# Optimization experiments

Measured on AMD Instinct MI355X. Metric: run time of the kernel, lower is better.

The kernel has to match this reference:

```python
import jax, jax.numpy as jnp
import numpy as np

B, N, DX, E, H, HD, KH, FF = 8, 8192, 2, 128, 8, 16, 32, 128
G1, G2, PMAX = 32, 32, 32


def _ln(x, g, b):
    mu = jnp.mean(x, axis=-1, keepdims=True)
    var = jnp.mean((x - mu) ** 2, axis=-1, keepdims=True)
    return (x - mu) * jax.lax.rsqrt(var + 1e-5) * g + b


def _cumcount_row(idx):
    # for each element, number of earlier elements with the same value (stable)
    n = idx.shape[0]
    order = jnp.argsort(idx)  # stable
    si = idx[order]
    ar = jnp.arange(n)
    is_start = jnp.concatenate([jnp.ones((1,), bool), si[1:] != si[:-1]])
    seg_start = jax.lax.associative_scan(jnp.maximum, jnp.where(is_start, ar, 0))
    return jnp.zeros(n, jnp.int32).at[order].set((ar - seg_start).astype(jnp.int32))


def _forward(x, z, latent, Wq, Wk, Wv, Wo, bo, kW1, kb1, kW2, kb2,
             lnq_g, lnq_b, lnk_g, lnk_b, ln2_g, ln2_b, fW1, fb1, fW2, fb2,
             grid_n1, grid_n2, max_patch, num_heads):
    Bb, Nn, dx = x.shape
    e = latent.shape[0]
    dims = (grid_n1, grid_n2)
    M = grid_n1 * grid_n2
    P = max_patch
    h = num_heads
    hd = Wq.shape[1] // h
    # grid range from data (margin = 0), regular grid via linspace
    mins = [jnp.min(x[:, :, i]) for i in range(dx)]
    maxs = [jnp.max(x[:, :, i]) for i in range(dx)]
    axes = [jnp.linspace(mins[i], maxs[i], dims[i]) for i in range(dx)]
    x_grid = jnp.stack(jnp.meshgrid(*axes, indexing="ij"), axis=-1)  # [G1,G2,dx]
    x_grid_flat = x_grid.reshape(M, dx)
    # nearest grid cell per point: regular grid -> per-dim rounding
    flat = None
    for i in range(dx):
        step = (maxs[i] - mins[i]) / (dims[i] - 1)
        ii = jnp.clip(jnp.round((x[..., i] - mins[i]) / step), 0, dims[i] - 1).astype(jnp.int32)
        flat = ii if flat is None else flat * dims[i] + ii
    cell = flat  # [B,N]
    cumc = jax.vmap(_cumcount_row)(cell)          # slot within cell
    slot = jnp.where(cumc < P, cumc, P)           # overflow -> dummy slot (dropped)
    bidx = jnp.broadcast_to(jnp.arange(Bb)[:, None], (Bb, Nn))
    # scatter points into per-cell padded neighbour sets [B, M, P, d]
    jx = jnp.zeros((Bb, M, P + 1, dx), x.dtype).at[bidx, cell, slot].set(x)[:, :, :P]
    jz = jnp.zeros((Bb, M, P + 1, e), z.dtype).at[bidx, cell, slot].set(z)[:, :, :P]
    msk = jnp.zeros((Bb, M, P + 1), bool).at[bidx, cell, slot].set(True)[:, :, :P]
    xg = jnp.broadcast_to(x_grid_flat[None], (Bb, M, dx))
    zg = jnp.broadcast_to(latent[None, None, :], (Bb, M, e))
    # concatenate_x_grid=True: grid token prepended, always attended
    joint_x = jnp.concatenate([xg[:, :, None, :], jx], axis=2).reshape(Bb * M, P + 1, dx)
    joint_z = jnp.concatenate([zg[:, :, None, :], jz], axis=2).reshape(Bb * M, P + 1, e)
    att_mask = jnp.concatenate([jnp.ones((Bb, M, 1), bool), msk], axis=2).reshape(Bb * M, P + 1)
    xq = xg.reshape(Bb * M, 1, dx)
    zq = zg.reshape(Bb * M, 1, e)
    T = Bb * M
    # masked translation-equivariant cross-attention (pre-norm layer)
    q = jnp.einsum("tqe,ef->tqf", _ln(zq, lnq_g, lnq_b), Wq).reshape(T, 1, h, hd)
    zk_n = _ln(joint_z, lnk_g, lnk_b)
    k = jnp.einsum("tke,ef->tkf", zk_n, Wk).reshape(T, P + 1, h, hd)
    v = jnp.einsum("tke,ef->tkf", zk_n, Wv).reshape(T, P + 1, h, hd)
    dots = jnp.einsum("tqhd,tkhd->thqk", q, k) / jnp.sqrt(jnp.asarray(hd, q.dtype))
    diff = joint_x[:, None, :, :] - xq[:, :, None, :]            # [T,1,P+1,dx]
    kb = jnp.maximum(diff @ kW1 + kb1, 0.0) @ kW2 + kb2          # kernel bias [T,1,P+1,h]
    dots = dots + jnp.transpose(kb, (0, 3, 1, 2))
    dots = jnp.where(att_mask[:, None, None, :], dots, -1e9)
    A = jax.nn.softmax(dots, axis=-1)                            # [T,h,1,P+1]
    out = jnp.einsum("thqk,tkhd->tqhd", A, v).reshape(T, 1, h * hd)
    z_new = zq + out @ Wo + bo
    z_new = z_new + (jnp.maximum(_ln(z_new, ln2_g, ln2_b) @ fW1 + fb1, 0.0) @ fW2 + fb2)
    x_new = jnp.einsum("tqk,tkd->tqd", jnp.mean(A, axis=1), joint_x)  # TE location update
    x_grid_out = x_new.reshape(Bb, grid_n1, grid_n2, dx)
    z_grid_out = z_new.reshape(Bb, grid_n1, grid_n2, e)
    return (x_grid_out, z_grid_out)


def setup_inputs():
    key = jax.random.key(0)
    ks = jax.random.split(key, 12)
    s = 0.05
    return {
        "x": jax.random.uniform(ks[0], (B, N, DX), jnp.float32),
        "z": jax.random.normal(ks[1], (B, N, E), jnp.float32),
        "grid_n1": G1, "grid_n2": G2, "max_patch": PMAX, "num_heads": H,
        "latent": jax.random.normal(ks[2], (E,), jnp.float32),
        "Wq": jax.random.normal(ks[3], (E, H * HD), jnp.float32) * s,
        "Wk": jax.random.normal(ks[4], (E, H * HD), jnp.float32) * s,
        "Wv": jax.random.normal(ks[5], (E, H * HD), jnp.float32) * s,
        "Wo": jax.random.normal(ks[6], (H * HD, E), jnp.float32) * s,
        "bo": jnp.zeros((E,), jnp.float32),
        "kW1": jax.random.normal(ks[7], (DX, KH), jnp.float32) * s,
        "kb1": jnp.zeros((KH,), jnp.float32),
        "kW2": jax.random.normal(ks[8], (KH, H), jnp.float32) * s,
        "kb2": jnp.zeros((H,), jnp.float32),
        "lnq_g": jnp.ones((E,), jnp.float32), "lnq_b": jnp.zeros((E,), jnp.float32),
        "lnk_g": jnp.ones((E,), jnp.float32), "lnk_b": jnp.zeros((E,), jnp.float32),
        "ln2_g": jnp.ones((E,), jnp.float32), "ln2_b": jnp.zeros((E,), jnp.float32),
        "fW1": jax.random.normal(ks[9], (E, FF), jnp.float32) * s,
        "fb1": jnp.zeros((FF,), jnp.float32),
        "fW2": jax.random.normal(ks[10], (FF, E), jnp.float32) * s,
        "fb2": jnp.zeros((E,), jnp.float32),
    }


def reference(x, z, grid_n1, grid_n2, max_patch, num_heads, latent, Wq, Wk, Wv, Wo, bo,
              kW1, kb1, kW2, kb2, lnq_g, lnq_b, lnk_g, lnk_b, ln2_g, ln2_b,
              fW1, fb1, fW2, fb2):
    return _forward(x, z, latent, Wq, Wk, Wv, Wo, bo, kW1, kb1, kW2, kb2,
                    lnq_g, lnq_b, lnk_g, lnk_b, ln2_g, ln2_b, fW1, fb1, fW2, fb2,
                    grid_n1, grid_n2, max_patch, num_heads)
```

## Files before the change

### kernel.cpp

```cpp
#include <hip/hip_runtime.h>
#include <stdint.h>

#define NB 8
#define NN 8192
#define NE 128
#define NH 8
#define NHD 16
#define NKH 32
#define NFF 128
#define NG 32
#define NM 1024
#define NP 32
#define NT 8192
#define NPTS 65536

typedef __attribute__((ext_vector_type(8))) short bf16x8_t;
typedef __attribute__((ext_vector_type(4))) float f32x4_t;

#define WS_MM      0
#define WS_D0      64
#define WS_Q       128
#define WS_VG      640
#define WS_PART    1152
#define WS_CNT     2048
#define WS_CELL    34816
#define WS_PIDX    296960
#define WS_WVT     1345536
#define WS_WOT     1411072
#define WS_FW1T    1443840
#define WS_FW2T    1476608
#define WS_WKQT    1509376
#define WS_SCORES  1513472
#define WS_KV      4194304

__device__ __forceinline__ unsigned short f2bf(float f) {
    unsigned u = __float_as_uint(f);
    u += 0x7FFFu + ((u >> 16) & 1u);
    return (unsigned short)(u >> 16);
}
__device__ __forceinline__ float bflo(unsigned w) { return __uint_as_float(w << 16); }
__device__ __forceinline__ float bfhi(unsigned w) { return __uint_as_float(w & 0xFFFF0000u); }

__global__ __launch_bounds__(256) void k_setup(
        const float* __restrict__ x,
        const float* __restrict__ Wk, const float* __restrict__ Wv, const float* __restrict__ Wo,
        const float* __restrict__ fW1, const float* __restrict__ fW2,
        const float* __restrict__ latent, const float* __restrict__ Wq,
        const float* __restrict__ lnq_g, const float* __restrict__ lnq_b,
        const float* __restrict__ lnk_g, const float* __restrict__ lnk_b,
        const float* __restrict__ kb1, const float* __restrict__ kW2, const float* __restrict__ kb2,
        int* __restrict__ cnt,
        unsigned short* __restrict__ WvT, unsigned short* __restrict__ WoT,
        unsigned short* __restrict__ fW1T, unsigned short* __restrict__ fW2T,
        float* __restrict__ ws_q, float* __restrict__ ws_vg, float* __restrict__ ws_d0,
        unsigned short* __restrict__ WkqT,
        float4* __restrict__ part) {
    int blk = blockIdx.x;
    int t = threadIdx.x;
    if (blk < 16) {
        __shared__ float s_t[64][65];
        const float* src; unsigned short* dst;
        int n0, k0;
        if (blk < 4) {
            int tn = blk >> 1, tk = blk & 1;
            n0 = tn * 64; k0 = tk * 64;
            src = Wv; dst = WvT;
        } else {
            int m = (blk - 4) >> 2, s4 = (blk - 4) & 3;
            int tn = s4 >> 1, tk = s4 & 1;
            n0 = tn * 64; k0 = tk * 64;
            src = (m == 0) ? Wo : (m == 1) ? fW1 : fW2;
            dst = (m == 0) ? WoT : (m == 1) ? fW1T : fW2T;
        }
        int tx = t & 63, ty = t >> 6;
        #pragma unroll
        for (int r = 0; r < 16; ++r) {
            int kr = r * 4 + ty;
            s_t[kr][tx] = src[(k0 + kr) * 128 + n0 + tx];
        }
        __syncthreads();
        #pragma unroll
        for (int r = 0; r < 16; ++r) {
            int nr = r * 4 + ty;
            dst[(n0 + nr) * 128 + k0 + tx] = f2bf(s_t[tx][nr]);
        }
    } else if (blk < 48) {
        int idx = (blk - 16) * 256 + t;
        cnt[idx] = 0;
    } else if (blk == 48) {
        __shared__ float s_qn[128], s_kn[128], s_q[128], s_kg[128];
        __shared__ float s_mu, s_rstd;
        if (t < 64) {
            float v0 = latent[t], v1 = latent[t + 64];
            float s = v0 + v1;
            for (int m = 32; m > 0; m >>= 1) s += __shfl_xor(s, m);
            float mu = s * (1.0f / 128.0f);
            float d0 = v0 - mu, d1 = v1 - mu;
            float q = d0 * d0 + d1 * d1;
            for (int m = 32; m > 0; m >>= 1) q += __shfl_xor(q, m);
            if (t == 0) { s_mu = mu; s_rstd = rsqrtf(q * (1.0f / 128.0f) + 1e-5f); }
        }
        __syncthreads();
        if (t < 128) {
            float nv = (latent[t] - s_mu) * s_rstd;
            s_qn[t] = nv * lnq_g[t] + lnq_b[t];
            s_kn[t] = nv * lnk_g[t] + lnk_b[t];
        }
        __syncthreads();
        if (t < 128) {
            float aq = 0.f, ak = 0.f, av = 0.f;
            for (int e = 0; e < 128; ++e) {
                aq += s_qn[e] * Wq[e * 128 + t];
                ak += s_kn[e] * Wk[e * 128 + t];
                av += s_kn[e] * Wv[e * 128 + t];
            }
            s_q[t] = aq; s_kg[t] = ak;
            ws_q[t] = aq; ws_vg[t] = av;
        }
        __syncthreads();
        if (t < 128) {
            const float* wr = Wk + t * 128;
            #pragma unroll
            for (int h = 0; h < 8; ++h) {
                float a = 0.f;
                #pragma unroll
                for (int d = 0; d < 16; ++d) a += wr[h * 16 + d] * s_q[h * 16 + d];
                WkqT[h * 128 + t] = f2bf(a * 0.25f);
                WkqT[(h + 8) * 128 + t] = 0;
            }
        }
        if (t < 8) {
            float acc = 0.f;
            for (int d = 0; d < 16; ++d) acc += s_q[t * 16 + d] * s_kg[t * 16 + d];
            float kb0 = kb2[t];
            for (int j = 0; j < 32; ++j) kb0 += fmaxf(kb1[j], 0.f) * kW2[j * 8 + t];
            ws_d0[t] = acc * 0.25f + kb0;
        }
    } else {
        __shared__ float s_red[4][4];
        int pb = blk - 49;
        const float4* xp = (const float4*)x + pb * 1024;
        float mn0 = 1e30f, mx0 = -1e30f, mn1 = 1e30f, mx1 = -1e30f;
        #pragma unroll
        for (int it = 0; it < 4; ++it) {
            float4 v = xp[it * 256 + t];
            mn0 = fminf(mn0, fminf(v.x, v.z)); mx0 = fmaxf(mx0, fmaxf(v.x, v.z));
            mn1 = fminf(mn1, fminf(v.y, v.w)); mx1 = fmaxf(mx1, fmaxf(v.y, v.w));
        }
        #pragma unroll
        for (int m = 32; m > 0; m >>= 1) {
            mn0 = fminf(mn0, __shfl_xor(mn0, m)); mx0 = fmaxf(mx0, __shfl_xor(mx0, m));
            mn1 = fminf(mn1, __shfl_xor(mn1, m)); mx1 = fmaxf(mx1, __shfl_xor(mx1, m));
        }
        int w = t >> 6;
        if ((t & 63) == 0) {
            s_red[w][0] = mn0; s_red[w][1] = mn1; s_red[w][2] = mx0; s_red[w][3] = mx1;
        }
        __syncthreads();
        if (t == 0) {
            float a0 = fminf(fminf(s_red[0][0], s_red[1][0]), fminf(s_red[2][0], s_red[3][0]));
            float a1 = fminf(fminf(s_red[0][1], s_red[1][1]), fminf(s_red[2][1], s_red[3][1]));
            float b0 = fmaxf(fmaxf(s_red[0][2], s_red[1][2]), fmaxf(s_red[2][2], s_red[3][2]));
            float b1 = fmaxf(fmaxf(s_red[0][3], s_red[1][3]), fmaxf(s_red[2][3], s_red[3][3]));
            part[pb] = make_float4(a0, a1, b0, b1);
        }
    }
}

__global__ __launch_bounds__(256) void k_binkv(
        const float* __restrict__ x, const float* __restrict__ z,
        const float4* __restrict__ part, float* __restrict__ mm,
        const float* __restrict__ lnk_g, const float* __restrict__ lnk_b,
        const unsigned short* __restrict__ WkqT,
        const float* __restrict__ kW1, const float* __restrict__ kb1,
        const float* __restrict__ kW2, const float* __restrict__ kb2,
        const unsigned short* __restrict__ WvT, unsigned short* __restrict__ kv,
        float* __restrict__ scores,
        int* __restrict__ cell, int* __restrict__ cnt, int* __restrict__ ptIdx) {
    int t = threadIdx.x;
    if (blockIdx.x >= 1024) {
        int l = t & 63;
        float mn0 = 1e30f, mn1 = 1e30f, mx0 = -1e30f, mx1 = -1e30f;
        if (l < 32) { float4 p = part[l]; mn0 = p.x; mn1 = p.y; mx0 = p.z; mx1 = p.w; }
        #pragma unroll
        for (int m = 32; m > 0; m >>= 1) {
            mn0 = fminf(mn0, __shfl_xor(mn0, m)); mx0 = fmaxf(mx0, __shfl_xor(mx0, m));
            mn1 = fminf(mn1, __shfl_xor(mn1, m)); mx1 = fmaxf(mx1, __shfl_xor(mx1, m));
        }
        if (blockIdx.x == 1024 && t == 0) {
            mm[0] = mn0; mm[1] = mn1; mm[2] = mx0; mm[3] = mx1;
        }
        int i = (blockIdx.x - 1024) * 256 + t;
        float st0 = (mx0 - mn0) / 31.0f, st1 = (mx1 - mn1) / 31.0f;
        float2 xv = ((const float2*)x)[i];
        int i0 = (int)rintf((xv.x - mn0) / st0); i0 = min(max(i0, 0), 31);
        int i1 = (int)rintf((xv.y - mn1) / st1); i1 = min(max(i1, 0), 31);
        int c = i0 * 32 + i1;
        cell[i] = c;
        int bb = i >> 13;
        int slot = atomicAdd(&cnt[bb * NM + c], 1);
        if (slot < NP) ptIdx[(bb * NM + c) * NP + slot] = i & (NN - 1);
        return;
    }
    __shared__ unsigned short s_zn[64][136];
    __shared__ unsigned short s_stage[4][16][68];
    int w = t >> 6, lane = t & 63;
    long base = (long)blockIdx.x * 64;
    int sub = lane >> 5;
    int lq = lane & 31;
    int mrow = lane & 15, quad = lane >> 4;

    float mn0 = 1e30f, mn1 = 1e30f, mx0 = -1e30f, mx1 = -1e30f;
    if (lane < 32) { float4 p = part[lane]; mn0 = p.x; mn1 = p.y; mx0 = p.z; mx1 = p.w; }
    #pragma unroll
    for (int m = 32; m > 0; m >>= 1) {
        mn0 = fminf(mn0, __shfl_xor(mn0, m)); mx0 = fmaxf(mx0, __shfl_xor(mx0, m));
        mn1 = fminf(mn1, __shfl_xor(mn1, m)); mx1 = fmaxf(mx1, __shfl_xor(mx1, m));
    }
    int ptl = w * 16 + mrow;
    float2 xv2 = ((const float2*)x)[base + ptl];

    int th = w >> 1, fh = w & 1;
    bf16x8_t afrag[4][4];
    #pragma unroll
    for (int j = 0; j < 4; ++j) {
        const unsigned short* ap = WvT + ((fh * 4 + j) * 16 + mrow) * 128 + quad * 8;
        #pragma unroll
        for (int kc = 0; kc < 4; ++kc)
            afrag[j][kc] = *(const bf16x8_t*)(ap + kc * 32);
    }
    bf16x8_t sfrag[4];
    #pragma unroll
    for (int kc = 0; kc < 4; ++kc)
        sfrag[kc] = *(const bf16x8_t*)(WkqT + mrow * 128 + kc * 32 + quad * 8);

    float4 g4 = ((const float4*)lnk_g)[lq];
    float4 b4 = ((const float4*)lnk_b)[lq];
    float4 v[8];
    #pragma unroll
    for (int i = 0; i < 8; ++i) {
        int pl = w * 16 + i * 2 + sub;
        v[i] = ((const float4*)z)[(base + pl) * 32 + lq];
    }
    #pragma unroll
    for (int i = 0; i < 8; ++i) {
        int pl = w * 16 + i * 2 + sub;
        float sum = v[i].x + v[i].y + v[i].z + v[i].w;
        float ssq = v[i].x * v[i].x + v[i].y * v[i].y + v[i].z * v[i].z + v[i].w * v[i].w;
        #pragma unroll
        for (int m = 1; m < 32; m <<= 1) {
            sum += __shfl_xor(sum, m);
            ssq += __shfl_xor(ssq, m);
        }
        float mu = sum * (1.0f / 128.0f);
        float var = fmaxf(ssq * (1.0f / 128.0f) - mu * mu, 0.0f);
        float rstd = rsqrtf(var + 1e-5f);
        float n0 = (v[i].x - mu) * rstd * g4.x + b4.x;
        float n1 = (v[i].y - mu) * rstd * g4.y + b4.y;
        float n2 = (v[i].z - mu) * rstd * g4.z + b4.z;
        float n3 = (v[i].w - mu) * rstd * g4.w + b4.w;
        unsigned d0 = (unsigned)f2bf(n0) | ((unsigned)f2bf(n1) << 16);
        unsigned d1 = (unsigned)f2bf(n2) | ((unsigned)f2bf(n3) << 16);
        *(uint2*)&s_zn[pl][lq * 4] = make_uint2(d0, d1);
    }
    __syncthreads();

    #pragma unroll
    for (int tau = 0; tau < 2; ++tau) {
        int trow = th * 32 + tau * 16;
        bf16x8_t bfrag[4];
        #pragma unroll
        for (int kc = 0; kc < 4; ++kc)
            bfrag[kc] = *(const bf16x8_t*)&s_zn[trow + mrow][kc * 32 + quad * 8];
        #pragma unroll
        for (int j = 0; j < 4; ++j) {
            f32x4_t acc = {0.f, 0.f, 0.f, 0.f};
            #pragma unroll
            for (int kc = 0; kc < 4; ++kc)
                acc = __builtin_amdgcn_mfma_f32_16x16x32_bf16(afrag[j][kc], bfrag[kc], acc, 0, 0, 0);
            unsigned d0 = (unsigned)f2bf(acc[0]) | ((unsigned)f2bf(acc[1]) << 16);
            unsigned d1 = (unsigned)f2bf(acc[2]) | ((unsigned)f2bf(acc[3]) << 16);
            *(uint2*)&s_stage[w][mrow][j * 16 + quad * 4] = make_uint2(d0, d1);
        }
        int tok = lane >> 3, u = lane & 7;
        long tk0 = base + trow;
        uint4 ra = *(const uint4*)&s_stage[w][tok][u * 8];
        *(uint4*)(kv + (tk0 + tok) * 128 + fh * 64 + u * 8) = ra;
        uint4 rb = *(const uint4*)&s_stage[w][tok + 8][u * 8];
        *(uint4*)(kv + (tk0 + tok + 8) * 128 + fh * 64 + u * 8) = rb;
    }

    f32x4_t sacc = {0.f, 0.f, 0.f, 0.f};
    {
        bf16x8_t sb[4];
        #pragma unroll
        for (int kc = 0; kc < 4; ++kc)
            sb[kc] = *(const bf16x8_t*)&s_zn[w * 16 + mrow][kc * 32 + quad * 8];
        #pragma unroll
        for (int kc = 0; kc < 4; ++kc)
            sacc = __builtin_amdgcn_mfma_f32_16x16x32_bf16(sfrag[kc], sb[kc], sacc, 0, 0, 0);
    }

    {
        float st0 = (mx0 - mn0) / 31.0f, st1 = (mx1 - mn1) / 31.0f;
        int i0 = (int)rintf((xv2.x - mn0) / st0); i0 = min(max(i0, 0), 31);
        int i1 = (int)rintf((xv2.y - mn1) / st1); i1 = min(max(i1, 0), 31);
        float cx0 = (i0 == 31) ? mx0 : mn0 + i0 * st0;
        float cx1 = (i1 == 31) ? mx1 : mn1 + i1 * st1;
        float d0 = xv2.x - cx0, d1 = xv2.y - cx1;
        float k0 = 0.f, k1 = 0.f, k2 = 0.f, k3 = 0.f, k4 = 0.f, k5 = 0.f, k6 = 0.f, k7 = 0.f;
        #pragma unroll
        for (int jj = 0; jj < 8; ++jj) {
            int j = quad * 8 + jj;
            float hj = fmaf(d0, kW1[j], fmaf(d1, kW1[32 + j], kb1[j]));
            hj = fmaxf(hj, 0.f);
            float4 w2a = *(const float4*)(kW2 + j * 8);
            float4 w2b = *(const float4*)(kW2 + j * 8 + 4);
            k0 = fmaf(hj, w2a.x, k0); k1 = fmaf(hj, w2a.y, k1);
            k2 = fmaf(hj, w2a.z, k2); k3 = fmaf(hj, w2a.w, k3);
            k4 = fmaf(hj, w2b.x, k4); k5 = fmaf(hj, w2b.y, k5);
            k6 = fmaf(hj, w2b.z, k6); k7 = fmaf(hj, w2b.w, k7);
        }
        k0 += __shfl_xor(k0, 16); k0 += __shfl_xor(k0, 32);
        k1 += __shfl_xor(k1, 16); k1 += __shfl_xor(k1, 32);
        k2 += __shfl_xor(k2, 16); k2 += __shfl_xor(k2, 32);
        k3 += __shfl_xor(k3, 16); k3 += __shfl_xor(k3, 32);
        k4 += __shfl_xor(k4, 16); k4 += __shfl_xor(k4, 32);
        k5 += __shfl_xor(k5, 16); k5 += __shfl_xor(k5, 32);
        k6 += __shfl_xor(k6, 16); k6 += __shfl_xor(k6, 32);
        k7 += __shfl_xor(k7, 16); k7 += __shfl_xor(k7, 32);
        if (quad == 0) {
            float4 kb2v = ((const float4*)kb2)[0];
            float4 o;
            o.x = sacc[0] + k0 + kb2v.x; o.y = sacc[1] + k1 + kb2v.y;
            o.z = sacc[2] + k2 + kb2v.z; o.w = sacc[3] + k3 + kb2v.w;
            *(float4*)(scores + ((size_t)(base + ptl)) * 8) = o;
        } else if (quad == 1) {
            float4 kb2v = ((const float4*)kb2)[1];
            float4 o;
            o.x = sacc[0] + k4 + kb2v.x; o.y = sacc[1] + k5 + kb2v.y;
            o.z = sacc[2] + k6 + kb2v.z; o.w = sacc[3] + k7 + kb2v.w;
            *(float4*)(scores + ((size_t)(base + ptl)) * 8 + 4) = o;
        }
    }
}

__global__ __launch_bounds__(256) void k_attn(const float* __restrict__ x,
        const int* __restrict__ cell, const int* __restrict__ cnt, int* __restrict__ ptIdx,
        const float* __restrict__ mm, const unsigned short* __restrict__ kv,
        const float* __restrict__ scores,
        const float* __restrict__ ws_vg, const float* __restrict__ ws_d0,
        const float* __restrict__ latent, const float* __restrict__ bo,
        const float* __restrict__ ln2_g, const float* __restrict__ ln2_b,
        const float* __restrict__ fb1, const float* __restrict__ fb2,
        const unsigned short* __restrict__ WoT, const unsigned short* __restrict__ fW1T,
        const unsigned short* __restrict__ fW2T,
        float* __restrict__ xout, float* __restrict__ zout) {
    __shared__ unsigned short s_a[16][136];
    __shared__ unsigned short s_a2[16][136];
    __shared__ float s_z[4][128];
    __shared__ float s_lat[128], s_g2[128], s_b2[128], s_fb1v[128], s_fb2v[128];
    int t = threadIdx.x;
    int l = t & 63;
    int w = t >> 6;
    int bm = blockIdx.x * 4 + w;
    int b = bm >> 10;
    int h = l >> 3, jp = l & 7;

    int craw = cnt[bm];
    if (t < 128) {
        s_lat[t] = latent[t] + bo[t];
        s_g2[t] = ln2_g[t]; s_b2[t] = ln2_b[t];
        s_fb1v[t] = fb1[t]; s_fb2v[t] = fb2[t];
    }

    float mn0 = mm[0], mn1 = mm[1], mx0 = mm[2], mx1 = mm[3];
    int i0 = (bm & 1023) >> 5, i1 = bm & 31;
    float st0 = (mx0 - mn0) / 31.0f, st1 = (mx1 - mn1) / 31.0f;
    float xg0 = (i0 == 31) ? mx0 : mn0 + i0 * st0;
    float xg1 = (i1 == 31) ? mx1 : mn1 + i1 * st1;
    int c = min(craw, NP);
    if (craw > NP) {
        int mycell = bm & 1023;
        const int* cb = cell + b * NN;
        int run = 0;
        for (int ch = 0; ch < NN / 64 && run < NP; ++ch) {
            int n = ch * 64 + l;
            bool match = (cb[n] == mycell);
            unsigned long long mask = __ballot(match);
            if (match) {
                int rank = run + __popcll(mask & ((1ull << l) - 1ull));
                if (rank < NP) ptIdx[bm * NP + rank] = n;
            }
            run += __popcll(mask);
        }
    }

    float vg0 = ws_vg[2 * l], vg1 = ws_vg[2 * l + 1];
    float ag = ws_d0[h];

    int idxreg = ptIdx[bm * NP + l] & (NN - 1);
    float2 xv = ((const float2*)x)[(size_t)b * NN + idxreg];
    float x0r = xv.x, x1r = xv.y;

    float areg[4];
    #pragma unroll
    for (int g = 0; g < 4; ++g) {
        int key = g * 8 + jp;
        int idxk = __shfl(idxreg, key);
        float sc = scores[((size_t)b * NN + idxk) * 8 + h];
        areg[g] = (key < c) ? sc : -1e30f;
    }
    unsigned vreg[16];
    #pragma unroll
    for (int k8 = 0; k8 < 16; ++k8) {
        int idxk = __shfl(idxreg, k8);
        unsigned vw = ((const unsigned*)kv)[((size_t)(b * NN + idxk) << 6) + l];
        vreg[k8] = (k8 < c) ? vw : 0u;
    }

    float mx = fmaxf(fmaxf(areg[0], areg[1]), fmaxf(areg[2], areg[3]));
    mx = fmaxf(mx, ag);
    mx = fmaxf(mx, __shfl_xor(mx, 1));
    mx = fmaxf(mx, __shfl_xor(mx, 2));
    mx = fmaxf(mx, __shfl_xor(mx, 4));
    float e0 = __expf(areg[0] - mx), e1 = __expf(areg[1] - mx);
    float e2 = __expf(areg[2] - mx), e3 = __expf(areg[3] - mx);
    float eg = __expf(ag - mx);
    float s = e0 + e1 + e2 + e3;
    s += __shfl_xor(s, 1);
    s += __shfl_xor(s, 2);
    s += __shfl_xor(s, 4);
    s += eg;
    float inv = 1.0f / s;

    float accA = eg * inv * vg0, accB = eg * inv * vg1;
    #pragma unroll
    for (int k8 = 0; k8 < 8; ++k8) {
        int src = (l & 56) | k8;
        float a0 = __shfl(e0, src) * inv;
        float a1 = __shfl(e1, src) * inv;
        unsigned vw0 = vreg[k8], vw1 = vreg[8 + k8];
        accA = fmaf(a0, bflo(vw0), accA); accB = fmaf(a0, bfhi(vw0), accB);
        accA = fmaf(a1, bflo(vw1), accA); accB = fmaf(a1, bfhi(vw1), accB);
    }
    if (c > 16) {
        #pragma unroll
        for (int k8 = 0; k8 < 8; ++k8) {
            int key2 = 16 + k8, key3 = 24 + k8;
            int idxk2 = __shfl(idxreg, key2);
            int idxk3 = __shfl(idxreg, key3);
            unsigned vw2 = ((const unsigned*)kv)[((size_t)(b * NN + idxk2) << 6) + l];
            unsigned vw3 = ((const unsigned*)kv)[((size_t)(b * NN + idxk3) << 6) + l];
            vw2 = (key2 < c) ? vw2 : 0u;
            vw3 = (key3 < c) ? vw3 : 0u;
            int src = (l & 56) | k8;
            float a2 = __shfl(e2, src) * inv;
            float a3 = __shfl(e3, src) * inv;
            accA = fmaf(a2, bflo(vw2), accA); accB = fmaf(a2, bfhi(vw2), accB);
            accA = fmaf(a3, bflo(vw3), accA); accB = fmaf(a3, bfhi(vw3), accB);
        }
    }
    unsigned ow = ((unsigned)f2bf(accB) << 16) | (unsigned)f2bf(accA);
    *(unsigned*)&s_a[w][2 * l] = ow;

    float s0 = e0 * inv, s1 = e1 * inv, s2 = e2 * inv, s3 = e3 * inv, sg = eg * inv;
    #pragma unroll
    for (int m = 8; m <= 32; m <<= 1) {
        s0 += __shfl_xor(s0, m); s1 += __shfl_xor(s1, m);
        s2 += __shfl_xor(s2, m); s3 += __shfl_xor(s3, m);
        sg += __shfl_xor(sg, m);
    }
    float px0 = 0.f, px1 = 0.f;
    {
        float xx0, xx1;
        xx0 = __shfl(x0r, jp);      xx1 = __shfl(x1r, jp);
        px0 = fmaf(s0, xx0, px0);   px1 = fmaf(s0, xx1, px1);
        xx0 = __shfl(x0r, jp + 8);  xx1 = __shfl(x1r, jp + 8);
        px0 = fmaf(s1, xx0, px0);   px1 = fmaf(s1, xx1, px1);
        xx0 = __shfl(x0r, jp + 16); xx1 = __shfl(x1r, jp + 16);
        px0 = fmaf(s2, xx0, px0);   px1 = fmaf(s2, xx1, px1);
        xx0 = __shfl(x0r, jp + 24); xx1 = __shfl(x1r, jp + 24);
        px0 = fmaf(s3, xx0, px0);   px1 = fmaf(s3, xx1, px1);
    }
    px0 += __shfl_xor(px0, 1); px1 += __shfl_xor(px1, 1);
    px0 += __shfl_xor(px0, 2); px1 += __shfl_xor(px1, 2);
    px0 += __shfl_xor(px0, 4); px1 += __shfl_xor(px1, 4);
    if (l == 0) {
        xout[bm * 2]     = (px0 + sg * xg0) * 0.125f;
        xout[bm * 2 + 1] = (px1 + sg * xg1) * 0.125f;
    }

    __syncthreads();
    int mrow = l & 15, quad = l >> 4;
    int base4 = blockIdx.x * 4;
    {
        bf16x8_t a[4];
        #pragma unroll
        for (int kc = 0; kc < 4; ++kc)
            a[kc] = *(const bf16x8_t*)&s_a[mrow][kc * 32 + quad * 8];
        #pragma unroll
        for (int cc = 0; cc < 2; ++cc) {
            int ct = w * 2 + cc;
            f32x4_t acc = {0.f, 0.f, 0.f, 0.f};
            const unsigned short* bp = WoT + (ct * 16 + mrow) * 128 + quad * 8;
            #pragma unroll
            for (int kc = 0; kc < 4; ++kc)
                acc = __builtin_amdgcn_mfma_f32_16x16x32_bf16(a[kc], *(const bf16x8_t*)(bp + kc * 32), acc, 0, 0, 0);
            if (quad == 0) {
                int f = ct * 16 + mrow;
                #pragma unroll
                for (int r = 0; r < 4; ++r) s_z[r][f] = acc[r] + s_lat[f];
            }
        }
    }
    __syncthreads();
    {
        float v0 = s_z[w][l], v1 = s_z[w][l + 64];
        float ssum = v0 + v1;
        #pragma unroll
        for (int m = 32; m > 0; m >>= 1) ssum += __shfl_xor(ssum, m);
        float mu = ssum * (1.0f / 128.0f);
        float d0 = v0 - mu, d1 = v1 - mu;
        float qq = d0 * d0 + d1 * d1;
        #pragma unroll
        for (int m = 32; m > 0; m >>= 1) qq += __shfl_xor(qq, m);
        float rstd = rsqrtf(qq * (1.0f / 128.0f) + 1e-5f);
        s_a2[w][l]      = f2bf(d0 * rstd * s_g2[l] + s_b2[l]);
        s_a2[w][l + 64] = f2bf(d1 * rstd * s_g2[l + 64] + s_b2[l + 64]);
    }
    __syncthreads();
    {
        bf16x8_t a[4];
        #pragma unroll
        for (int kc = 0; kc < 4; ++kc)
            a[kc] = *(const bf16x8_t*)&s_a2[mrow][kc * 32 + quad * 8];
        #pragma unroll
        for (int cc = 0; cc < 2; ++cc) {
            int ct = w * 2 + cc;
            f32x4_t acc = {0.f, 0.f, 0.f, 0.f};
            const unsigned short* bp = fW1T + (ct * 16 + mrow) * 128 + quad * 8;
            #pragma unroll
            for (int kc = 0; kc < 4; ++kc)
                acc = __builtin_amdgcn_mfma_f32_16x16x32_bf16(a[kc], *(const bf16x8_t*)(bp + kc * 32), acc, 0, 0, 0);
            if (quad == 0) {
                int f = ct * 16 + mrow;
                #pragma unroll
                for (int r = 0; r < 4; ++r)
                    s_a[r][f] = f2bf(fmaxf(acc[r] + s_fb1v[f], 0.f));
            }
        }
    }
    __syncthreads();
    {
        bf16x8_t a[4];
        #pragma unroll
        for (int kc = 0; kc < 4; ++kc)
            a[kc] = *(const bf16x8_t*)&s_a[mrow][kc * 32 + quad * 8];
        #pragma unroll
        for (int cc = 0; cc < 2; ++cc) {
            int ct = w * 2 + cc;
            f32x4_t acc = {0.f, 0.f, 0.f, 0.f};
            const unsigned short* bp = fW2T + (ct * 16 + mrow) * 128 + quad * 8;
            #pragma unroll
            for (int kc = 0; kc < 4; ++kc)
                acc = __builtin_amdgcn_mfma_f32_16x16x32_bf16(a[kc], *(const bf16x8_t*)(bp + kc * 32), acc, 0, 0, 0);
            if (quad == 0) {
                int f = ct * 16 + mrow;
                #pragma unroll
                for (int r = 0; r < 4; ++r)
                    zout[(base4 + r) * 128 + f] = s_z[r][f] + acc[r] + s_fb2v[f];
            }
        }
    }
}

extern "C" void kernel_launch(void* const* d_in, const int* in_sizes, int n_in,
                              void* d_out, int out_size, void* d_ws, size_t ws_size,
                              hipStream_t stream) {
    const float* x     = (const float*)d_in[0];
    const float* z     = (const float*)d_in[1];
    const float* latent= (const float*)d_in[6];
    const float* Wq    = (const float*)d_in[7];
    const float* Wk    = (const float*)d_in[8];
    const float* Wv    = (const float*)d_in[9];
    const float* Wo    = (const float*)d_in[10];
    const float* bo    = (const float*)d_in[11];
    const float* kW1   = (const float*)d_in[12];
    const float* kb1   = (const float*)d_in[13];
    const float* kW2   = (const float*)d_in[14];
    const float* kb2   = (const float*)d_in[15];
    const float* lnq_g = (const float*)d_in[16];
    const float* lnq_b = (const float*)d_in[17];
    const float* lnk_g = (const float*)d_in[18];
    const float* lnk_b = (const float*)d_in[19];
    const float* ln2_g = (const float*)d_in[20];
    const float* ln2_b = (const float*)d_in[21];
    const float* fW1   = (const float*)d_in[22];
    const float* fb1   = (const float*)d_in[23];
    const float* fW2   = (const float*)d_in[24];
    const float* fb2   = (const float*)d_in[25];

    uint8_t* ws = (uint8_t*)d_ws;
    float* mm     = (float*)(ws + WS_MM);
    float* ws_d0  = (float*)(ws + WS_D0);
    float* ws_q   = (float*)(ws + WS_Q);
    float* ws_vg  = (float*)(ws + WS_VG);
    float4* part  = (float4*)(ws + WS_PART);
    int* cnt      = (int*)(ws + WS_CNT);
    int* cell     = (int*)(ws + WS_CELL);
    int* ptIdx    = (int*)(ws + WS_PIDX);
    unsigned short* WvT  = (unsigned short*)(ws + WS_WVT);
    unsigned short* WoT  = (unsigned short*)(ws + WS_WOT);
    unsigned short* fW1T = (unsigned short*)(ws + WS_FW1T);
    unsigned short* fW2T = (unsigned short*)(ws + WS_FW2T);
    unsigned short* WkqT = (unsigned short*)(ws + WS_WKQT);
    float* scores = (float*)(ws + WS_SCORES);
    unsigned short* kv   = (unsigned short*)(ws + WS_KV);

    float* xout = (float*)d_out;
    float* zout = (float*)d_out + 16384;

    k_setup <<<81,   256, 0, stream>>>(x, Wk, Wv, Wo, fW1, fW2, latent, Wq,
                                       lnq_g, lnq_b, lnk_g, lnk_b, kb1, kW2, kb2,
                                       cnt, WvT, WoT, fW1T, fW2T, ws_q, ws_vg, ws_d0,
                                       WkqT, part);
    k_binkv <<<1280, 256, 0, stream>>>(x, z, part, mm, lnk_g, lnk_b, WkqT,
                                       kW1, kb1, kW2, kb2, WvT, kv, scores,
                                       cell, cnt, ptIdx);
    k_attn  <<<2048, 256, 0, stream>>>(x, cell, cnt, ptIdx, mm, kv, scores,
                                       ws_vg, ws_d0,
                                       latent, bo, ln2_g, ln2_b, fb1, fb2,
                                       WoT, fW1T, fW2T, xout, zout);
}
```

Before: 182.6 us.

## Scatter V, scores and coordinates directly into per-cell slot layout during projection

Binning now happens inside the projection kernel. Each point atomically claims a slot in its cell, and its V row, head scores and coordinates are written straight into a dense per-cell padded buffer. This replaces the token-ordered kv/scores arrays plus the ptIdx index list. The attention kernel then reads contiguous per-cell slots instead of gathering through indices, and the separate binning blocks are removed from the launch. The cost is a large sparse padded workspace, and the stable-order fallback for cells holding more than max_patch points is gone, so which points are kept in an overflowing cell depends on atomic ordering.

Result: no change. 184.5 us (+1.0%).

```diff
diff --git a/kernel.cpp b/kernel.cpp
--- a/kernel.cpp
+++ b/kernel.cpp
@@ -23,15 +23,14 @@
 #define WS_VG      640
 #define WS_PART    1152
 #define WS_CNT     2048
-#define WS_CELL    34816
-#define WS_PIDX    296960
-#define WS_WVT     1345536
-#define WS_WOT     1411072
-#define WS_FW1T    1443840
-#define WS_FW2T    1476608
-#define WS_WKQT    1509376
-#define WS_SCORES  1513472
-#define WS_KV      4194304
+#define WS_WVT     34816
+#define WS_WOT     67584
+#define WS_FW1T    100352
+#define WS_FW2T    133120
+#define WS_WKQT    165888
+#define WS_XD      169984
+#define WS_SD      2267136
+#define WS_VD      10655744
 
 __device__ __forceinline__ unsigned short f2bf(float f) {
     unsigned u = __float_as_uint(f);
@@ -174,36 +173,13 @@
         const unsigned short* __restrict__ WkqT,
         const float* __restrict__ kW1, const float* __restrict__ kb1,
         const float* __restrict__ kW2, const float* __restrict__ kb2,
-        const unsigned short* __restrict__ WvT, unsigned short* __restrict__ kv,
-        float* __restrict__ scores,
-        int* __restrict__ cell, int* __restrict__ cnt, int* __restrict__ ptIdx) {
-    int t = threadIdx.x;
-    if (blockIdx.x >= 1024) {
-        int l = t & 63;
-        float mn0 = 1e30f, mn1 = 1e30f, mx0 = -1e30f, mx1 = -1e30f;
-        if (l < 32) { float4 p = part[l]; mn0 = p.x; mn1 = p.y; mx0 = p.z; mx1 = p.w; }
-        #pragma unroll
-        for (int m = 32; m > 0; m >>= 1) {
-            mn0 = fminf(mn0, __shfl_xor(mn0, m)); mx0 = fmaxf(mx0, __shfl_xor(mx0, m));
-            mn1 = fminf(mn1, __shfl_xor(mn1, m)); mx1 = fmaxf(mx1, __shfl_xor(mx1, m));
-        }
-        if (blockIdx.x == 1024 && t == 0) {
-            mm[0] = mn0; mm[1] = mn1; mm[2] = mx0; mm[3] = mx1;
-        }
-        int i = (blockIdx.x - 1024) * 256 + t;
-        float st0 = (mx0 - mn0) / 31.0f, st1 = (mx1 - mn1) / 31.0f;
-        float2 xv = ((const float2*)x)[i];
-        int i0 = (int)rintf((xv.x - mn0) / st0); i0 = min(max(i0, 0), 31);
-        int i1 = (int)rintf((xv.y - mn1) / st1); i1 = min(max(i1, 0), 31);
-        int c = i0 * 32 + i1;
-        cell[i] = c;
-        int bb = i >> 13;
-        int slot = atomicAdd(&cnt[bb * NM + c], 1);
-        if (slot < NP) ptIdx[(bb * NM + c) * NP + slot] = i & (NN - 1);
-        return;
-    }
+        const unsigned short* __restrict__ WvT,
+        unsigned short* __restrict__ vd, float* __restrict__ sd, float2* __restrict__ xd,
+        int* __restrict__ cnt) {
     __shared__ unsigned short s_zn[64][136];
     __shared__ unsigned short s_stage[4][16][68];
+    __shared__ int s_dsl[64];
+    int t = threadIdx.x;
     int w = t >> 6, lane = t & 63;
     long base = (long)blockIdx.x * 64;
     int sub = lane >> 5;
@@ -216,6 +192,9 @@
     for (int m = 32; m > 0; m >>= 1) {
         mn0 = fminf(mn0, __shfl_xor(mn0, m)); mx0 = fmaxf(mx0, __shfl_xor(mx0, m));
         mn1 = fminf(mn1, __shfl_xor(mn1, m)); mx1 = fmaxf(mx1, __shfl_xor(mx1, m));
+    }
+    if (blockIdx.x == 0 && t == 0) {
+        mm[0] = mn0; mm[1] = mn1; mm[2] = mx0; mm[3] = mx1;
     }
     int ptl = w * 16 + mrow;
     float2 xv2 = ((const float2*)x)[base + ptl];
@@ -263,6 +242,17 @@
         unsigned d1 = (unsigned)f2bf(n2) | ((unsigned)f2bf(n3) << 16);
         *(uint2*)&s_zn[pl][lq * 4] = make_uint2(d0, d1);
     }
+
+    float st0 = (mx0 - mn0) / 31.0f, st1 = (mx1 - mn1) / 31.0f;
+    int i0 = (int)rintf((xv2.x - mn0) / st0); i0 = min(max(i0, 0), 31);
+    int i1 = (int)rintf((xv2.y - mn1) / st1); i1 = min(max(i1, 0), 31);
+    if (quad == 0) {
+        long gi = base + ptl;
+        int bb = (int)(gi >> 13);
+        int cellc = (bb << 10) + i0 * 32 + i1;
+        int slot = atomicAdd(&cnt[cellc], 1);
+        s_dsl[ptl] = (slot < NP) ? ((cellc << 5) + slot) : -1;
+    }
     __syncthreads();
 
     #pragma unroll
@@ -283,11 +273,12 @@
             *(uint2*)&s_stage[w][mrow][j * 16 + quad * 4] = make_uint2(d0, d1);
         }
         int tok = lane >> 3, u = lane & 7;
-        long tk0 = base + trow;
+        int dsA = s_dsl[trow + tok];
+        int dsB = s_dsl[trow + tok + 8];
         uint4 ra = *(const uint4*)&s_stage[w][tok][u * 8];
-        *(uint4*)(kv + (tk0 + tok) * 128 + fh * 64 + u * 8) = ra;
         uint4 rb = *(const uint4*)&s_stage[w][tok + 8][u * 8];
-        *(uint4*)(kv + (tk0 + tok + 8) * 128 + fh * 64 + u * 8) = rb;
+        if (dsA >= 0) *(uint4*)(vd + (size_t)dsA * 128 + fh * 64 + u * 8) = ra;
+        if (dsB >= 0) *(uint4*)(vd + (size_t)dsB * 128 + fh * 64 + u * 8) = rb;
     }
 
     f32x4_t sacc = {0.f, 0.f, 0.f, 0.f};
@@ -302,9 +293,6 @@
     }
 
     {
-        float st0 = (mx0 - mn0) / 31.0f, st1 = (mx1 - mn1) / 31.0f;
-        int i0 = (int)rintf((xv2.x - mn0) / st0); i0 = min(max(i0, 0), 31);
-        int i1 = (int)rintf((xv2.y - mn1) / st1); i1 = min(max(i1, 0), 31);
         float cx0 = (i0 == 31) ? mx0 : mn0 + i0 * st0;
         float cx1 = (i1 == 31) ? mx1 : mn1 + i1 * st1;
         float d0 = xv2.x - cx0, d1 = xv2.y - cx1;
@@ -329,26 +317,31 @@
         k5 += __shfl_xor(k5, 16); k5 += __shfl_xor(k5, 32);
         k6 += __shfl_xor(k6, 16); k6 += __shfl_xor(k6, 32);
         k7 += __shfl_xor(k7, 16); k7 += __shfl_xor(k7, 32);
-        if (quad == 0) {
-            float4 kb2v = ((const float4*)kb2)[0];
-            float4 o;
-            o.x = sacc[0] + k0 + kb2v.x; o.y = sacc[1] + k1 + kb2v.y;
-            o.z = sacc[2] + k2 + kb2v.z; o.w = sacc[3] + k3 + kb2v.w;
-            *(float4*)(scores + ((size_t)(base + ptl)) * 8) = o;
-        } else if (quad == 1) {
-            float4 kb2v = ((const float4*)kb2)[1];
-            float4 o;
-            o.x = sacc[0] + k4 + kb2v.x; o.y = sacc[1] + k5 + kb2v.y;
-            o.z = sacc[2] + k6 + kb2v.z; o.w = sacc[3] + k7 + kb2v.w;
-            *(float4*)(scores + ((size_t)(base + ptl)) * 8 + 4) = o;
+        int dslv = s_dsl[ptl];
+        if (dslv >= 0) {
+            if (quad == 0) {
+                float4 kb2v = ((const float4*)kb2)[0];
+                float4 o;
+                o.x = sacc[0] + k0 + kb2v.x; o.y = sacc[1] + k1 + kb2v.y;
+                o.z = sacc[2] + k2 + kb2v.z; o.w = sacc[3] + k3 + kb2v.w;
+                *(float4*)(sd + (size_t)dslv * 8) = o;
+            } else if (quad == 1) {
+                float4 kb2v = ((const float4*)kb2)[1];
+                float4 o;
+                o.x = sacc[0] + k4 + kb2v.x; o.y = sacc[1] + k5 + kb2v.y;
+                o.z = sacc[2] + k6 + kb2v.z; o.w = sacc[3] + k7 + kb2v.w;
+                *(float4*)(sd + (size_t)dslv * 8 + 4) = o;
+            } else if (quad == 2) {
+                xd[dslv] = xv2;
+            }
         }
     }
 }
 
-__global__ __launch_bounds__(256) void k_attn(const float* __restrict__ x,
-        const int* __restrict__ cell, const int* __restrict__ cnt, int* __restrict__ ptIdx,
-        const float* __restrict__ mm, const unsigned short* __restrict__ kv,
-        const float* __restrict__ scores,
+__global__ __launch_bounds__(256) void k_attn(
+        const int* __restrict__ cnt, const float* __restrict__ mm,
+        const unsigned short* __restrict__ vd, const float* __restrict__ sd,
+        const float2* __restrict__ xd,
         const float* __restrict__ ws_vg, const float* __restrict__ ws_d0,
         const float* __restrict__ latent, const float* __restrict__ bo,
         const float* __restrict__ ln2_g, const float* __restrict__ ln2_b,
@@ -364,7 +357,6 @@
     int l = t & 63;
     int w = t >> 6;
     int bm = blockIdx.x * 4 + w;
-    int b = bm >> 10;
     int h = l >> 3, jp = l & 7;
 
     int craw = cnt[bm];
@@ -374,50 +366,46 @@
         s_fb1v[t] = fb1[t]; s_fb2v[t] = fb2[t];
     }
 
+    size_t db = (size_t)bm << 5;
+
+    float scv[4];
+    float2 xv4[4];
+    #pragma unroll
+    for (int g = 0; g < 4; ++g) {
+        scv[g] = sd[(db + g * 8 + jp) * 8 + h];
+        xv4[g] = xd[db + g * 8 + jp];
+    }
+    unsigned vreg[16];
+    const unsigned* vrow = (const unsigned*)vd + db * 64;
+    #pragma unroll
+    for (int k = 0; k < 8; ++k) vreg[k] = vrow[(size_t)k * 64 + l];
+
+    int c = min(craw, NP);
+    #pragma unroll
+    for (int k = 0; k < 8; ++k) vreg[k] = (k < c) ? vreg[k] : 0u;
+    if (c > 8) {
+        #pragma unroll
+        for (int k = 8; k < 16; ++k) {
+            unsigned vw = vrow[(size_t)k * 64 + l];
+            vreg[k] = (k < c) ? vw : 0u;
+        }
+    } else {
+        #pragma unroll
+        for (int k = 8; k < 16; ++k) vreg[k] = 0u;
+    }
+
     float mn0 = mm[0], mn1 = mm[1], mx0 = mm[2], mx1 = mm[3];
     int i0 = (bm & 1023) >> 5, i1 = bm & 31;
     float st0 = (mx0 - mn0) / 31.0f, st1 = (mx1 - mn1) / 31.0f;
     float xg0 = (i0 == 31) ? mx0 : mn0 + i0 * st0;
     float xg1 = (i1 == 31) ? mx1 : mn1 + i1 * st1;
-    int c = min(craw, NP);
-    if (craw > NP) {
-        int mycell = bm & 1023;
-        const int* cb = cell + b * NN;
-        int run = 0;
-        for (int ch = 0; ch < NN / 64 && run < NP; ++ch) {
-            int n = ch * 64 + l;
-            bool match = (cb[n] == mycell);
-            unsigned long long mask = __ballot(match);
-            if (match) {
-                int rank = run + __popcll(mask & ((1ull << l) - 1ull));
-                if (rank < NP) ptIdx[bm * NP + rank] = n;
-            }
-            run += __popcll(mask);
-        }
-    }
-
     float vg0 = ws_vg[2 * l], vg1 = ws_vg[2 * l + 1];
     float ag = ws_d0[h];
 
-    int idxreg = ptIdx[bm * NP + l] & (NN - 1);
-    float2 xv = ((const float2*)x)[(size_t)b * NN + idxreg];
-    float x0r = xv.x, x1r = xv.y;
-
     float areg[4];
     #pragma unroll
-    for (int g = 0; g < 4; ++g) {
-        int key = g * 8 + jp;
-        int idxk = __shfl(idxreg, key);
-        float sc = scores[((size_t)b * NN + idxk) * 8 + h];
-        areg[g] = (key < c) ? sc : -1e30f;
-    }
-    unsigned vreg[16];
-    #pragma unroll
-    for (int k8 = 0; k8 < 16; ++k8) {
-        int idxk = __shfl(idxreg, k8);
-        unsigned vw = ((const unsigned*)kv)[((size_t)(b * NN + idxk) << 6) + l];
-        vreg[k8] = (k8 < c) ? vw : 0u;
-    }
+    for (int g = 0; g < 4; ++g)
+        areg[g] = (g * 8 + jp < c) ? scv[g] : -1e30f;
 
     float mx = fmaxf(fmaxf(areg[0], areg[1]), fmaxf(areg[2], areg[3]));
     mx = fmaxf(mx, ag);
@@ -448,10 +436,8 @@
         #pragma unroll
         for (int k8 = 0; k8 < 8; ++k8) {
             int key2 = 16 + k8, key3 = 24 + k8;
-            int idxk2 = __shfl(idxreg, key2);
-            int idxk3 = __shfl(idxreg, key3);
-            unsigned vw2 = ((const unsigned*)kv)[((size_t)(b * NN + idxk2) << 6) + l];
-            unsigned vw3 = ((const unsigned*)kv)[((size_t)(b * NN + idxk3) << 6) + l];
+            unsigned vw2 = vrow[(size_t)key2 * 64 + l];
+            unsigned vw3 = vrow[(size_t)key3 * 64 + l];
             vw2 = (key2 < c) ? vw2 : 0u;
             vw3 = (key3 < c) ? vw3 : 0u;
             int src = (l & 56) | k8;
@@ -473,15 +459,11 @@
     }
     float px0 = 0.f, px1 = 0.f;
     {
-        float xx0, xx1;
-        xx0 = __shfl(x0r, jp);      xx1 = __shfl(x1r, jp);
-        px0 = fmaf(s0, xx0, px0);   px1 = fmaf(s0, xx1, px1);
-        xx0 = __shfl(x0r, jp + 8);  xx1 = __shfl(x1r, jp + 8);
-        px0 = fmaf(s1, xx0, px0);   px1 = fmaf(s1, xx1, px1);
-        xx0 = __shfl(x0r, jp + 16); xx1 = __shfl(x1r, jp + 16);
-        px0 = fmaf(s2, xx0, px0);   px1 = fmaf(s2, xx1, px1);
-        xx0 = __shfl(x0r, jp + 24); xx1 = __shfl(x1r, jp + 24);
-        px0 = fmaf(s3, xx0, px0);   px1 = fmaf(s3, xx1, px1);
+        bool v0 = (jp < c), v1 = (8 + jp < c), v2 = (16 + jp < c), v3 = (24 + jp < c);
+        px0 = fmaf(s0, v0 ? xv4[0].x : 0.f, px0);  px1 = fmaf(s0, v0 ? xv4[0].y : 0.f, px1);
+        px0 = fmaf(s1, v1 ? xv4[1].x : 0.f, px0);  px1 = fmaf(s1, v1 ? xv4[1].y : 0.f, px1);
+        px0 = fmaf(s2, v2 ? xv4[2].x : 0.f, px0);  px1 = fmaf(s2, v2 ? xv4[2].y : 0.f, px1);
+        px0 = fmaf(s3, v3 ? xv4[3].x : 0.f, px0);  px1 = fmaf(s3, v3 ? xv4[3].y : 0.f, px1);
     }
     px0 += __shfl_xor(px0, 1); px1 += __shfl_xor(px1, 1);
     px0 += __shfl_xor(px0, 2); px1 += __shfl_xor(px1, 2);
@@ -608,15 +590,14 @@
     float* ws_vg  = (float*)(ws + WS_VG);
     float4* part  = (float4*)(ws + WS_PART);
     int* cnt      = (int*)(ws + WS_CNT);
-    int* cell     = (int*)(ws + WS_CELL);
-    int* ptIdx    = (int*)(ws + WS_PIDX);
     unsigned short* WvT  = (unsigned short*)(ws + WS_WVT);
     unsigned short* WoT  = (unsigned short*)(ws + WS_WOT);
     unsigned short* fW1T = (unsigned short*)(ws + WS_FW1T);
     unsigned short* fW2T = (unsigned short*)(ws + WS_FW2T);
     unsigned short* WkqT = (unsigned short*)(ws + WS_WKQT);
-    float* scores = (float*)(ws + WS_SCORES);
-    unsigned short* kv   = (unsigned short*)(ws + WS_KV);
+    float2* xd    = (float2*)(ws + WS_XD);
+    float* sd     = (float*)(ws + WS_SD);
+    unsigned short* vd = (unsigned short*)(ws + WS_VD);
 
     float* xout = (float*)d_out;
     float* zout = (float*)d_out + 16384;
@@ -625,10 +606,10 @@
                                        lnq_g, lnq_b, lnk_g, lnk_b, kb1, kW2, kb2,
                                        cnt, WvT, WoT, fW1T, fW2T, ws_q, ws_vg, ws_d0,
                                        WkqT, part);
-    k_binkv <<<1280, 256, 0, stream>>>(x, z, part, mm, lnk_g, lnk_b, WkqT,
-                                       kW1, kb1, kW2, kb2, WvT, kv, scores,
-                                       cell, cnt, ptIdx);
-    k_attn  <<<2048, 256, 0, stream>>>(x, cell, cnt, ptIdx, mm, kv, scores,
+    k_binkv <<<1024, 256, 0, stream>>>(x, z, part, mm, lnk_g, lnk_b, WkqT,
+                                       kW1, kb1, kW2, kb2, WvT,
+                                       vd, sd, xd, cnt);
+    k_attn  <<<2048, 256, 0, stream>>>(cnt, mm, vd, sd, xd,
                                        ws_vg, ws_d0,
                                        latent, bo, ln2_g, ln2_b, fb1, fb2,
                                        WoT, fW1T, fW2T, xout, zout);
```
